# Performance work log

Measured on AMD Instinct MI355X. Metric: run time of the kernel, lower is better.

## Reference

```python
import jax, jax.numpy as jnp
import numpy as np

B, T, F, H, O = 256, 128, 128, 1024, 128


def setup_inputs() -> dict:
    key = jax.random.key(0)
    ks = jax.random.split(key, 16)
    s = 0.02  # small init scale to keep gates in a sane range
    return {
        "batch": jax.random.normal(ks[0], (B, T, F), jnp.float32),
        "Wih0": jax.random.normal(ks[1], (4 * H, F), jnp.float32) * s,
        "Whh0": jax.random.normal(ks[2], (4 * H, H), jnp.float32) * s,
        "bih0": jax.random.normal(ks[3], (4 * H,), jnp.float32) * s,
        "bhh0": jax.random.normal(ks[4], (4 * H,), jnp.float32) * s,
        "Wih1": jax.random.normal(ks[5], (4 * H, H), jnp.float32) * s,
        "Whh1": jax.random.normal(ks[6], (4 * H, H), jnp.float32) * s,
        "bih1": jax.random.normal(ks[7], (4 * H,), jnp.float32) * s,
        "bhh1": jax.random.normal(ks[8], (4 * H,), jnp.float32) * s,
        "h00": jax.random.normal(ks[9], (B, H), jnp.float32) * s,
        "c00": jax.random.normal(ks[10], (B, H), jnp.float32) * s,
        "h01": jax.random.normal(ks[11], (B, H), jnp.float32) * s,
        "c01": jax.random.normal(ks[12], (B, H), jnp.float32) * s,
        "Wout": jax.random.normal(ks[13], (O, T * H), jnp.float32) * 0.01,
        "bout": jax.random.normal(ks[14], (O,), jnp.float32) * 0.01,
    }


def _lstm_cell(x, h, c, Wih, Whh, bih, bhh):
    # torch.nn.LSTMCell: gates = x @ Wih.T + bih + h @ Whh.T + bhh, chunks i,f,g,o
    gates = x @ Wih.T + bih + h @ Whh.T + bhh  # [B, 4H]
    i, f, g, o = jnp.split(gates, 4, axis=-1)
    c_new = jax.nn.sigmoid(f) * c + jax.nn.sigmoid(i) * jnp.tanh(g)
    h_new = jax.nn.sigmoid(o) * jnp.tanh(c_new)
    return h_new, c_new


def reference(batch, Wih0, Whh0, bih0, bhh0, Wih1, Whh1, bih1, bhh1,
              h00, c00, h01, c01, Wout, bout):
    # Faithful to original: batch.view(T, B, -1) is a pure RESHAPE, not transpose.
    x = batch.reshape(T, B, F)

    def step(carry, xt):
        h0, c0, h1, c1 = carry
        h0, c0 = _lstm_cell(xt, h0, c0, Wih0, Whh0, bih0, bhh0)
        h1, c1 = _lstm_cell(h0, h1, c1, Wih1, Whh1, bih1, bhh1)
        return (h0, c0, h1, c1), h1

    _, outs = jax.lax.scan(step, (h00, c00, h01, c01), x)  # outs: [T, B, H]
    # Faithful: io.view(B, T, -1) then Flatten -> pure reshape to [B, T*H]
    flat = outs.reshape(B, T * H)
    return flat @ Wout.T + bout  # [B, O]
```

## Files before the change

### kernel.cpp

```cpp
#include <hip/hip_runtime.h>
#include <hip/hip_cooperative_groups.h>

namespace cg = cooperative_groups;

typedef __attribute__((ext_vector_type(8))) short short8;
typedef __attribute__((ext_vector_type(4))) float f32x4;

#define NBATCH 256
#define NSTEP  128
#define NFEAT  128
#define NHID   1024
#define NOUT   128
#define KOUT   131072
#define NBLK   256

#define W0H_OFF 0
#define W1_OFF  32768
#define CH_OFF  98304
#define SMEM_BYTES 163840

#define MFMA __builtin_amdgcn_mfma_f32_16x16x32_bf16

__device__ __forceinline__ unsigned short f2bf(float f){
  unsigned u = __float_as_uint(f);
  u += 0x7fffu + ((u >> 16) & 1u);
  return (unsigned short)(u >> 16);
}
__device__ __forceinline__ float sigf(float x){
  x = fminf(fmaxf(x, -30.f), 30.f);
  return 1.f / (1.f + __expf(-x));
}
__device__ __forceinline__ float tanhf_(float x){
  x = fminf(fmaxf(x, -15.f), 15.f);
  float e = __expf(2.f * x);
  return (e - 1.f) / (e + 1.f);
}

struct Params {
  const float *batch,*Wih0,*Whh0,*bih0,*bhh0,*Wih1,*Whh1,*bih1,*bhh1,*h00,*c00,*h01,*c01,*Wout,*bout;
  float *out;
  unsigned short *h0b,*h1b,*outs,*xbf;
  float *partial;
  unsigned *ctr;
};

__device__ __forceinline__ short8 ld8(const unsigned short* p){
  return *(const short8*)p;
}
__device__ __forceinline__ short8 ld8f(const float* p){
  f32x4 a = *(const f32x4*)p;
  f32x4 b = *(const f32x4*)(p + 4);
  short8 r;
  r[0]=(short)f2bf(a[0]); r[1]=(short)f2bf(a[1]); r[2]=(short)f2bf(a[2]); r[3]=(short)f2bf(a[3]);
  r[4]=(short)f2bf(b[0]); r[5]=(short)f2bf(b[1]); r[6]=(short)f2bf(b[2]); r[7]=(short)f2bf(b[3]);
  return r;
}

__device__ __forceinline__ void dma16(const void* g, void* l){
  __builtin_amdgcn_global_load_lds((const __attribute__((address_space(1))) unsigned int*)g,
                                   (__attribute__((address_space(3))) unsigned int*)l, 16, 0, 0);
}

__device__ __forceinline__ void slim_bar(unsigned* c, int tid){
  __syncthreads();
  if (tid == 0) {
    __builtin_amdgcn_fence(__ATOMIC_RELEASE, "agent");
    __hip_atomic_fetch_add(c, 1u, __ATOMIC_RELAXED, __HIP_MEMORY_SCOPE_AGENT);
    while (__hip_atomic_load(c, __ATOMIC_RELAXED, __HIP_MEMORY_SCOPE_AGENT) < (unsigned)NBLK)
      __builtin_amdgcn_s_sleep(2);
  }
  __syncthreads();
  __builtin_amdgcn_fence(__ATOMIC_ACQUIRE, "agent");
}

__global__ void __launch_bounds__(512, 2) lstm_all(Params a)
{
  extern __shared__ char smem[];
  const int bx = blockIdx.x, tid = threadIdx.x;
  const int gtid = bx * 512 + tid, nthr = gridDim.x * 512;
  const int w = tid >> 6, l = tid & 63, lo = l & 15, hi = l >> 4;
  const int klane = hi * 8;
  const int dR  = l >> 2;
  const int dgo = (((l & 3) ^ ((l >> 3) & 3)) & 3) * 8;

  if (bx == 0) for (int i = tid; i < 192; i += 512) a.ctr[i] = 0;
  for (int item = tid; item < 128 * 16; item += 512) {
    int g = item >> 4, lr = item & 15;
    int r = 16 * bx + lr, orig = (r & 3) * NHID + (r >> 2);
    *(short8*)(smem + W0H_OFF + item * 16) = ld8f(a.Whh0 + (size_t)orig * NHID + g * 8);
  }
  for (int item = tid; item < 256 * 16; item += 512) {
    int g = item >> 4, lr = item & 15;
    int r = 16 * bx + lr, orig = (r & 3) * NHID + (r >> 2);
    int k = g * 8;
    const float* src = (k < NHID) ? a.Wih1 + (size_t)orig * NHID + k
                                  : a.Whh1 + (size_t)orig * NHID + (k - NHID);
    *(short8*)(smem + W1_OFF + item * 16) = ld8f(src);
  }
  short8 wx[4];
  {
    int r = 16 * bx + lo, orig = (r & 3) * NHID + (r >> 2);
    const float* s = a.Wih0 + (size_t)orig * NFEAT + klane;
    #pragma unroll
    for (int i = 0; i < 4; i++) wx[i] = ld8f(s + i * 32);
  }
  for (int i = gtid; i < NBATCH * NHID; i += nthr) {
    a.h0b[NBATCH * NHID + i] = f2bf(a.h00[i]);
    a.h1b[NBATCH * NHID + i] = f2bf(a.h01[i]);
  }
  for (int i = gtid; i < NSTEP * NBATCH * NFEAT / 8; i += nthr)
    *(short8*)(a.xbf + (size_t)i * 8) = ld8f(a.batch + (size_t)i * 8);

  const int j = 4 * bx + hi;
  float b0r[4], b1r[4];
  #pragma unroll
  for (int q = 0; q < 4; q++) {
    b0r[q] = a.bih0[q * NHID + j] + a.bhh0[q * NHID + j];
    b1r[q] = a.bih1[q * NHID + j] + a.bhh1[q * NHID + j];
  }
  const int m0 = w * 32 + lo, m1 = m0 + 16;
  float c0r[2], c1r[2];
  c0r[0] = a.c00[(size_t)m0 * NHID + j]; c0r[1] = a.c00[(size_t)m1 * NHID + j];
  c1r[0] = a.c01[(size_t)m0 * NHID + j]; c1r[1] = a.c01[(size_t)m1 * NHID + j];
  __syncthreads();
  cg::this_grid().sync();

  const int rdo = lo * 64 + ((hi ^ ((lo >> 1) & 3)) << 4);
  for (int p = 0; p <= NSTEP; p++) {
    const int wpar = p & 1, rp = wpar ^ 1;
    const unsigned short* h0p = a.h0b + (size_t)rp   * NBATCH * NHID;
    const unsigned short* h1p = a.h1b + (size_t)wpar * NBATCH * NHID;
    const int t0 = (p < NSTEP) ? p : (NSTEP - 1);
    const unsigned short* xA  = a.xbf + (size_t)t0 * NBATCH * NFEAT + (size_t)(w * 32 + dR) * NFEAT + dgo;
    const unsigned short* h0A = h0p + (size_t)(w * 32 + dR) * NHID + dgo;
    const unsigned short* h1A = h1p + (size_t)(w * 32 + dR) * NHID + dgo;

    auto issue = [&](int cc){
      char* base = smem + CH_OFF + (cc & 3) * 16384 + w * 2048;
      if (cc < 4) {
        int ko = cc * 32;
        dma16(xA + ko, base); dma16(xA + 16 * NFEAT + ko, base + 1024);
      } else if (cc < 36) {
        int ko = (cc - 4) * 32;
        dma16(h0A + ko, base); dma16(h0A + 16 * NHID + ko, base + 1024);
      } else {
        int ko = (cc - 36) * 32;
        dma16(h1A + ko, base); dma16(h1A + 16 * NHID + ko, base + 1024);
      }
    };

    f32x4 l0a0 = {0.f,0.f,0.f,0.f}, l0a1 = {0.f,0.f,0.f,0.f};
    f32x4 l1a0 = {0.f,0.f,0.f,0.f}, l1a1 = {0.f,0.f,0.f,0.f};

    issue(0); issue(1); issue(2);

    #pragma unroll
    for (int c = 0; c < 68; ++c) {
      if      (c <= 65) asm volatile("s_waitcnt vmcnt(4)\n\ts_barrier" ::: "memory");
      else if (c == 66) asm volatile("s_waitcnt vmcnt(2)\n\ts_barrier" ::: "memory");
      else              asm volatile("s_waitcnt vmcnt(0)\n\ts_barrier" ::: "memory");
      if (c + 3 < 68) issue(c + 3);

      const char* cb = smem + CH_OFF + (c & 3) * 16384 + w * 2048;
      short8 a0 = *(const short8*)(cb + rdo);
      short8 a1 = *(const short8*)(cb + 1024 + rdo);

      if (c < 4) {
        l0a0 = MFMA(wx[c], a0, l0a0, 0,0,0); l0a1 = MFMA(wx[c], a1, l0a1, 0,0,0);
      } else if (c < 36) {
        int g = (c - 4) * 4 + hi;
        short8 w0f = *(const short8*)(smem + W0H_OFF + g * 256 + lo * 16);
        short8 w1f = *(const short8*)(smem + W1_OFF  + g * 256 + lo * 16);
        l0a0 = MFMA(w0f, a0, l0a0, 0,0,0); l0a1 = MFMA(w0f, a1, l0a1, 0,0,0);
        l1a0 = MFMA(w1f, a0, l1a0, 0,0,0); l1a1 = MFMA(w1f, a1, l1a1, 0,0,0);
      } else {
        int g = 128 + (c - 36) * 4 + hi;
        short8 wf = *(const short8*)(smem + W1_OFF + g * 256 + lo * 16);
        l1a0 = MFMA(wf, a0, l1a0, 0,0,0); l1a1 = MFMA(wf, a1, l1a1, 0,0,0);
      }
    }

    if (p < NSTEP) {
      unsigned short* ho = a.h0b + (size_t)wpar * NBATCH * NHID;
      float cn0 = sigf(l0a0[1] + b0r[1]) * c0r[0] + sigf(l0a0[0] + b0r[0]) * tanhf_(l0a0[2] + b0r[2]);
      c0r[0] = cn0;
      ho[(size_t)m0 * NHID + j] = f2bf(sigf(l0a0[3] + b0r[3]) * tanhf_(cn0));
      float cn1 = sigf(l0a1[1] + b0r[1]) * c0r[1] + sigf(l0a1[0] + b0r[0]) * tanhf_(l0a1[2] + b0r[2]);
      c0r[1] = cn1;
      ho[(size_t)m1 * NHID + j] = f2bf(sigf(l0a1[3] + b0r[3]) * tanhf_(cn1));
    }
    if (p >= 1) {
      unsigned short* h1o = a.h1b + (size_t)rp * NBATCH * NHID;
      unsigned short* oo  = a.outs + (size_t)(p - 1) * NBATCH * NHID;
      float cn0 = sigf(l1a0[1] + b1r[1]) * c1r[0] + sigf(l1a0[0] + b1r[0]) * tanhf_(l1a0[2] + b1r[2]);
      c1r[0] = cn0;
      unsigned short u0 = f2bf(sigf(l1a0[3] + b1r[3]) * tanhf_(cn0));
      h1o[(size_t)m0 * NHID + j] = u0; oo[(size_t)m0 * NHID + j] = u0;
      float cn1 = sigf(l1a1[1] + b1r[1]) * c1r[1] + sigf(l1a1[0] + b1r[0]) * tanhf_(l1a1[2] + b1r[2]);
      c1r[1] = cn1;
      unsigned short u1 = f2bf(sigf(l1a1[3] + b1r[3]) * tanhf_(cn1));
      h1o[(size_t)m1 * NHID + j] = u1; oo[(size_t)m1 * NHID + j] = u1;
    }
    slim_bar(a.ctr + p, tid);
  }

  cg::this_grid().sync();

  {
    int fnt = bx & 3, kc = bx >> 2;
    f32x4 facc[2][2];
    #pragma unroll
    for (int i = 0; i < 2; i++) { facc[i][0] = (f32x4)(0.f); facc[i][1] = (f32x4)(0.f); }
    const int kbase = kc * 2048;
    #pragma unroll 2
    for (int kk = 0; kk < 64; kk++) {
      short8 wf0 = ld8f(a.Wout + (size_t)(fnt * 32 +  0 + lo) * KOUT + kbase + kk * 32 + klane);
      short8 wf1 = ld8f(a.Wout + (size_t)(fnt * 32 + 16 + lo) * KOUT + kbase + kk * 32 + klane);
      #pragma unroll
      for (int mf = 0; mf < 2; mf++) {
        const unsigned short* ip = a.outs + (size_t)((w * 2 + mf) * 16 + lo) * KOUT + kbase + kk * 32 + klane;
        short8 af = ld8(ip);
        facc[mf][0] = MFMA(wf0, af, facc[mf][0], 0,0,0);
        facc[mf][1] = MFMA(wf1, af, facc[mf][1], 0,0,0);
      }
    }
    #pragma unroll
    for (int mf = 0; mf < 2; mf++)
      #pragma unroll
      for (int nf = 0; nf < 2; nf++)
        #pragma unroll
        for (int r = 0; r < 4; r++) {
          int o_loc = nf * 16 + 4 * hi + r;
          int i = (w * 2 + mf) * 16 + lo;
          a.partial[(size_t)(kc * 4 + fnt) * 8192 + o_loc * 256 + i] = facc[mf][nf][r];
        }
  }
  cg::this_grid().sync();

  for (int idx = gtid; idx < NBATCH * NOUT; idx += nthr) {
    int i = idx >> 7, o = idx & 127;
    float s = a.bout[o];
    #pragma unroll 4
    for (int kc2 = 0; kc2 < 64; kc2++)
      s += a.partial[(size_t)(kc2 * 4 + (o >> 5)) * 8192 + (o & 31) * 256 + i];
    a.out[idx] = s;
  }
}

extern "C" void kernel_launch(void* const* d_in, const int* in_sizes, int n_in,
                              void* d_out, int out_size, void* d_ws, size_t ws_size,
                              hipStream_t stream)
{
  (void)in_sizes; (void)n_in; (void)out_size; (void)ws_size;
  Params a;
  a.batch = (const float*)d_in[0];  a.Wih0 = (const float*)d_in[1];
  a.Whh0  = (const float*)d_in[2];  a.bih0 = (const float*)d_in[3];
  a.bhh0  = (const float*)d_in[4];  a.Wih1 = (const float*)d_in[5];
  a.Whh1  = (const float*)d_in[6];  a.bih1 = (const float*)d_in[7];
  a.bhh1  = (const float*)d_in[8];  a.h00  = (const float*)d_in[9];
  a.c00   = (const float*)d_in[10]; a.h01  = (const float*)d_in[11];
  a.c01   = (const float*)d_in[12]; a.Wout = (const float*)d_in[13];
  a.bout  = (const float*)d_in[14];
  a.out   = (float*)d_out;

  char* ws = (char*)d_ws;
  size_t off = 0;
  auto carve = [&](size_t bytes) { char* p = ws + off; off += (bytes + 255) & ~(size_t)255; return p; };
  a.h0b     = (unsigned short*)carve((size_t)2 * NBATCH * NHID * 2);
  a.h1b     = (unsigned short*)carve((size_t)2 * NBATCH * NHID * 2);
  a.outs    = (unsigned short*)carve((size_t)NSTEP * NBATCH * NHID * 2);
  a.xbf     = (unsigned short*)carve((size_t)NSTEP * NBATCH * NFEAT * 2);
  a.partial = (float*)carve((size_t)256 * 8192 * 4);
  a.ctr     = (unsigned*)carve((size_t)256 * 4);

  hipFuncSetAttribute((const void*)lstm_all, hipFuncAttributeMaxDynamicSharedMemorySize, SMEM_BYTES);

  void* kargs[] = { &a };
  hipLaunchCooperativeKernel((void*)lstm_all, dim3(256), dim3(512), kargs, SMEM_BYTES, stream);
}
```

Measured before the change: 5.527 ms.

## Replace LDS DMA staging of activations with direct register prefetch pipeline

Drops the global_load_lds ring buffer in shared memory, along with its per-chunk waitcnt and s_barrier sync. Each wave now loads its own A fragments straight from global memory into a register ring that runs 7 chunks ahead. This cuts LDS use and the block-wide barriers inside the hot loop. The cost is more VGPRs for the 16 prefetched short8 values, compiler-managed wait counts, and possibly less coalesced global loads. Occupancy is pinned to 2 waves per EU.

```diff
diff --git a/kernel.cpp b/kernel.cpp
--- a/kernel.cpp
+++ b/kernel.cpp
@@ -16,8 +16,7 @@
 
 #define W0H_OFF 0
 #define W1_OFF  32768
-#define CH_OFF  98304
-#define SMEM_BYTES 163840
+#define SMEM_BYTES 98304
 
 #define MFMA __builtin_amdgcn_mfma_f32_16x16x32_bf16
 
@@ -56,11 +55,6 @@
   return r;
 }
 
-__device__ __forceinline__ void dma16(const void* g, void* l){
-  __builtin_amdgcn_global_load_lds((const __attribute__((address_space(1))) unsigned int*)g,
-                                   (__attribute__((address_space(3))) unsigned int*)l, 16, 0, 0);
-}
-
 __device__ __forceinline__ void slim_bar(unsigned* c, int tid){
   __syncthreads();
   if (tid == 0) {
@@ -73,15 +67,14 @@
   __builtin_amdgcn_fence(__ATOMIC_ACQUIRE, "agent");
 }
 
-__global__ void __launch_bounds__(512, 2) lstm_all(Params a)
+__attribute__((amdgpu_waves_per_eu(2, 2)))
+__global__ void __launch_bounds__(512) lstm_all(Params a)
 {
   extern __shared__ char smem[];
   const int bx = blockIdx.x, tid = threadIdx.x;
   const int gtid = bx * 512 + tid, nthr = gridDim.x * 512;
   const int w = tid >> 6, l = tid & 63, lo = l & 15, hi = l >> 4;
   const int klane = hi * 8;
-  const int dR  = l >> 2;
-  const int dgo = (((l & 3) ^ ((l >> 3) & 3)) & 3) * 8;
 
   if (bx == 0) for (int i = tid; i < 192; i += 512) a.ctr[i] = 0;
   for (int item = tid; item < 128 * 16; item += 512) {
@@ -125,45 +118,41 @@
   __syncthreads();
   cg::this_grid().sync();
 
-  const int rdo = lo * 64 + ((hi ^ ((lo >> 1) & 3)) << 4);
   for (int p = 0; p <= NSTEP; p++) {
     const int wpar = p & 1, rp = wpar ^ 1;
     const unsigned short* h0p = a.h0b + (size_t)rp   * NBATCH * NHID;
     const unsigned short* h1p = a.h1b + (size_t)wpar * NBATCH * NHID;
     const int t0 = (p < NSTEP) ? p : (NSTEP - 1);
-    const unsigned short* xA  = a.xbf + (size_t)t0 * NBATCH * NFEAT + (size_t)(w * 32 + dR) * NFEAT + dgo;
-    const unsigned short* h0A = h0p + (size_t)(w * 32 + dR) * NHID + dgo;
-    const unsigned short* h1A = h1p + (size_t)(w * 32 + dR) * NHID + dgo;
-
-    auto issue = [&](int cc){
-      char* base = smem + CH_OFF + (cc & 3) * 16384 + w * 2048;
-      if (cc < 4) {
-        int ko = cc * 32;
-        dma16(xA + ko, base); dma16(xA + 16 * NFEAT + ko, base + 1024);
-      } else if (cc < 36) {
-        int ko = (cc - 4) * 32;
-        dma16(h0A + ko, base); dma16(h0A + 16 * NHID + ko, base + 1024);
-      } else {
-        int ko = (cc - 36) * 32;
-        dma16(h1A + ko, base); dma16(h1A + 16 * NHID + ko, base + 1024);
-      }
+    const unsigned short* xP0  = a.xbf + (size_t)t0 * NBATCH * NFEAT + (size_t)m0 * NFEAT + klane;
+    const unsigned short* xP1  = xP0 + (size_t)16 * NFEAT;
+    const unsigned short* h0P0 = h0p + (size_t)m0 * NHID + klane;
+    const unsigned short* h0P1 = h0P0 + (size_t)16 * NHID;
+    const unsigned short* h1P0 = h1p + (size_t)m0 * NHID + klane;
+    const unsigned short* h1P1 = h1P0 + (size_t)16 * NHID;
+
+    auto lda0 = [&](int cc){
+      return (cc < 4) ? ld8(xP0 + cc * 32)
+           : (cc < 36) ? ld8(h0P0 + (cc - 4) * 32)
+                       : ld8(h1P0 + (cc - 36) * 32);
+    };
+    auto lda1 = [&](int cc){
+      return (cc < 4) ? ld8(xP1 + cc * 32)
+           : (cc < 36) ? ld8(h0P1 + (cc - 4) * 32)
+                       : ld8(h1P1 + (cc - 36) * 32);
     };
 
     f32x4 l0a0 = {0.f,0.f,0.f,0.f}, l0a1 = {0.f,0.f,0.f,0.f};
     f32x4 l1a0 = {0.f,0.f,0.f,0.f}, l1a1 = {0.f,0.f,0.f,0.f};
 
-    issue(0); issue(1); issue(2);
+    short8 ra[8], rb[8];
+    #pragma unroll
+    for (int q = 0; q < 7; q++) { ra[q] = lda0(q); rb[q] = lda1(q); }
 
     #pragma unroll
     for (int c = 0; c < 68; ++c) {
-      if      (c <= 65) asm volatile("s_waitcnt vmcnt(4)\n\ts_barrier" ::: "memory");
-      else if (c == 66) asm volatile("s_waitcnt vmcnt(2)\n\ts_barrier" ::: "memory");
-      else              asm volatile("s_waitcnt vmcnt(0)\n\ts_barrier" ::: "memory");
-      if (c + 3 < 68) issue(c + 3);
-
-      const char* cb = smem + CH_OFF + (c & 3) * 16384 + w * 2048;
-      short8 a0 = *(const short8*)(cb + rdo);
-      short8 a1 = *(const short8*)(cb + 1024 + rdo);
+      if (c + 7 < 68) { ra[(c + 7) & 7] = lda0(c + 7); rb[(c + 7) & 7] = lda1(c + 7); }
+      short8 a0 = ra[c & 7];
+      short8 a1 = rb[c & 7];
 
       if (c < 4) {
         l0a0 = MFMA(wx[c], a0, l0a0, 0,0,0); l0a1 = MFMA(wx[c], a1, l0a1, 0,0,0);
```

Result: slower. 8.210 ms (+48.5%).

## Double waves per block and give each wave a private DMA ring without barriers

Applied to the files above, without the earlier changes.

Each block now runs 1024 threads (16 waves), and each wave owns 16 batch rows instead of 32. The per-step MFMA chain per wave is halved, and the output projection is split the same way. Each wave gets its own 4-slot LDS ring for the x/h0/h1 chunks, so the block-wide s_barrier in the K loop is replaced by a per-wave vmcnt wait. The aim is to shorten the latency-bound critical path of each recurrent step. The cost is register pressure under 1024-thread launch bounds and more waves contending for LDS and the global barrier.

```diff
diff --git a/kernel.cpp b/kernel.cpp
--- a/kernel.cpp
+++ b/kernel.cpp
@@ -73,23 +73,23 @@
   __builtin_amdgcn_fence(__ATOMIC_ACQUIRE, "agent");
 }
 
-__global__ void __launch_bounds__(512, 2) lstm_all(Params a)
+__global__ void __launch_bounds__(1024, 4) lstm_all(Params a)
 {
   extern __shared__ char smem[];
   const int bx = blockIdx.x, tid = threadIdx.x;
-  const int gtid = bx * 512 + tid, nthr = gridDim.x * 512;
+  const int gtid = bx * 1024 + tid, nthr = gridDim.x * 1024;
   const int w = tid >> 6, l = tid & 63, lo = l & 15, hi = l >> 4;
   const int klane = hi * 8;
   const int dR  = l >> 2;
   const int dgo = (((l & 3) ^ ((l >> 3) & 3)) & 3) * 8;
 
-  if (bx == 0) for (int i = tid; i < 192; i += 512) a.ctr[i] = 0;
-  for (int item = tid; item < 128 * 16; item += 512) {
+  if (bx == 0) for (int i = tid; i < 192; i += 1024) a.ctr[i] = 0;
+  for (int item = tid; item < 128 * 16; item += 1024) {
     int g = item >> 4, lr = item & 15;
     int r = 16 * bx + lr, orig = (r & 3) * NHID + (r >> 2);
     *(short8*)(smem + W0H_OFF + item * 16) = ld8f(a.Whh0 + (size_t)orig * NHID + g * 8);
   }
-  for (int item = tid; item < 256 * 16; item += 512) {
+  for (int item = tid; item < 256 * 16; item += 1024) {
     int g = item >> 4, lr = item & 15;
     int r = 16 * bx + lr, orig = (r & 3) * NHID + (r >> 2);
     int k = g * 8;
@@ -112,94 +112,78 @@
     *(short8*)(a.xbf + (size_t)i * 8) = ld8f(a.batch + (size_t)i * 8);
 
   const int j = 4 * bx + hi;
+  const int m0 = w * 16 + lo;
   float b0r[4], b1r[4];
   #pragma unroll
   for (int q = 0; q < 4; q++) {
     b0r[q] = a.bih0[q * NHID + j] + a.bhh0[q * NHID + j];
     b1r[q] = a.bih1[q * NHID + j] + a.bhh1[q * NHID + j];
   }
-  const int m0 = w * 32 + lo, m1 = m0 + 16;
-  float c0r[2], c1r[2];
-  c0r[0] = a.c00[(size_t)m0 * NHID + j]; c0r[1] = a.c00[(size_t)m1 * NHID + j];
-  c1r[0] = a.c01[(size_t)m0 * NHID + j]; c1r[1] = a.c01[(size_t)m1 * NHID + j];
+  float c0r = a.c00[(size_t)m0 * NHID + j];
+  float c1r = a.c01[(size_t)m0 * NHID + j];
   __syncthreads();
   cg::this_grid().sync();
 
+  char* ring = smem + CH_OFF + w * 4096;
   const int rdo = lo * 64 + ((hi ^ ((lo >> 1) & 3)) << 4);
   for (int p = 0; p <= NSTEP; p++) {
     const int wpar = p & 1, rp = wpar ^ 1;
     const unsigned short* h0p = a.h0b + (size_t)rp   * NBATCH * NHID;
     const unsigned short* h1p = a.h1b + (size_t)wpar * NBATCH * NHID;
     const int t0 = (p < NSTEP) ? p : (NSTEP - 1);
-    const unsigned short* xA  = a.xbf + (size_t)t0 * NBATCH * NFEAT + (size_t)(w * 32 + dR) * NFEAT + dgo;
-    const unsigned short* h0A = h0p + (size_t)(w * 32 + dR) * NHID + dgo;
-    const unsigned short* h1A = h1p + (size_t)(w * 32 + dR) * NHID + dgo;
+    const unsigned short* xA  = a.xbf + (size_t)t0 * NBATCH * NFEAT + (size_t)(w * 16 + dR) * NFEAT + dgo;
+    const unsigned short* h0A = h0p + (size_t)(w * 16 + dR) * NHID + dgo;
+    const unsigned short* h1A = h1p + (size_t)(w * 16 + dR) * NHID + dgo;
 
     auto issue = [&](int cc){
-      char* base = smem + CH_OFF + (cc & 3) * 16384 + w * 2048;
-      if (cc < 4) {
-        int ko = cc * 32;
-        dma16(xA + ko, base); dma16(xA + 16 * NFEAT + ko, base + 1024);
-      } else if (cc < 36) {
-        int ko = (cc - 4) * 32;
-        dma16(h0A + ko, base); dma16(h0A + 16 * NHID + ko, base + 1024);
-      } else {
-        int ko = (cc - 36) * 32;
-        dma16(h1A + ko, base); dma16(h1A + 16 * NHID + ko, base + 1024);
-      }
+      char* base = ring + (cc & 3) * 1024;
+      if      (cc < 4)  dma16(xA  + cc * 32,        base);
+      else if (cc < 36) dma16(h0A + (cc - 4) * 32,  base);
+      else              dma16(h1A + (cc - 36) * 32, base);
     };
 
-    f32x4 l0a0 = {0.f,0.f,0.f,0.f}, l0a1 = {0.f,0.f,0.f,0.f};
-    f32x4 l1a0 = {0.f,0.f,0.f,0.f}, l1a1 = {0.f,0.f,0.f,0.f};
+    f32x4 l0a0 = {0.f,0.f,0.f,0.f};
+    f32x4 l1a0 = {0.f,0.f,0.f,0.f};
 
     issue(0); issue(1); issue(2);
 
     #pragma unroll
     for (int c = 0; c < 68; ++c) {
-      if      (c <= 65) asm volatile("s_waitcnt vmcnt(4)\n\ts_barrier" ::: "memory");
-      else if (c == 66) asm volatile("s_waitcnt vmcnt(2)\n\ts_barrier" ::: "memory");
-      else              asm volatile("s_waitcnt vmcnt(0)\n\ts_barrier" ::: "memory");
+      if      (c <= 65) asm volatile("s_waitcnt vmcnt(2)" ::: "memory");
+      else if (c == 66) asm volatile("s_waitcnt vmcnt(1)" ::: "memory");
+      else              asm volatile("s_waitcnt vmcnt(0)" ::: "memory");
       if (c + 3 < 68) issue(c + 3);
 
-      const char* cb = smem + CH_OFF + (c & 3) * 16384 + w * 2048;
-      short8 a0 = *(const short8*)(cb + rdo);
-      short8 a1 = *(const short8*)(cb + 1024 + rdo);
+      short8 a0 = *(const short8*)(ring + (c & 3) * 1024 + rdo);
 
       if (c < 4) {
-        l0a0 = MFMA(wx[c], a0, l0a0, 0,0,0); l0a1 = MFMA(wx[c], a1, l0a1, 0,0,0);
+        l0a0 = MFMA(wx[c], a0, l0a0, 0,0,0);
       } else if (c < 36) {
         int g = (c - 4) * 4 + hi;
         short8 w0f = *(const short8*)(smem + W0H_OFF + g * 256 + lo * 16);
         short8 w1f = *(const short8*)(smem + W1_OFF  + g * 256 + lo * 16);
-        l0a0 = MFMA(w0f, a0, l0a0, 0,0,0); l0a1 = MFMA(w0f, a1, l0a1, 0,0,0);
-        l1a0 = MFMA(w1f, a0, l1a0, 0,0,0); l1a1 = MFMA(w1f, a1, l1a1, 0,0,0);
+        l0a0 = MFMA(w0f, a0, l0a0, 0,0,0);
+        l1a0 = MFMA(w1f, a0, l1a0, 0,0,0);
       } else {
         int g = 128 + (c - 36) * 4 + hi;
         short8 wf = *(const short8*)(smem + W1_OFF + g * 256 + lo * 16);
-        l1a0 = MFMA(wf, a0, l1a0, 0,0,0); l1a1 = MFMA(wf, a1, l1a1, 0,0,0);
+        l1a0 = MFMA(wf, a0, l1a0, 0,0,0);
       }
     }
 
     if (p < NSTEP) {
       unsigned short* ho = a.h0b + (size_t)wpar * NBATCH * NHID;
-      float cn0 = sigf(l0a0[1] + b0r[1]) * c0r[0] + sigf(l0a0[0] + b0r[0]) * tanhf_(l0a0[2] + b0r[2]);
-      c0r[0] = cn0;
-      ho[(size_t)m0 * NHID + j] = f2bf(sigf(l0a0[3] + b0r[3]) * tanhf_(cn0));
-      float cn1 = sigf(l0a1[1] + b0r[1]) * c0r[1] + sigf(l0a1[0] + b0r[0]) * tanhf_(l0a1[2] + b0r[2]);
-      c0r[1] = cn1;
-      ho[(size_t)m1 * NHID + j] = f2bf(sigf(l0a1[3] + b0r[3]) * tanhf_(cn1));
+      float cn = sigf(l0a0[1] + b0r[1]) * c0r + sigf(l0a0[0] + b0r[0]) * tanhf_(l0a0[2] + b0r[2]);
+      c0r = cn;
+      ho[(size_t)m0 * NHID + j] = f2bf(sigf(l0a0[3] + b0r[3]) * tanhf_(cn));
     }
     if (p >= 1) {
       unsigned short* h1o = a.h1b + (size_t)rp * NBATCH * NHID;
       unsigned short* oo  = a.outs + (size_t)(p - 1) * NBATCH * NHID;
-      float cn0 = sigf(l1a0[1] + b1r[1]) * c1r[0] + sigf(l1a0[0] + b1r[0]) * tanhf_(l1a0[2] + b1r[2]);
-      c1r[0] = cn0;
-      unsigned short u0 = f2bf(sigf(l1a0[3] + b1r[3]) * tanhf_(cn0));
-      h1o[(size_t)m0 * NHID + j] = u0; oo[(size_t)m0 * NHID + j] = u0;
-      float cn1 = sigf(l1a1[1] + b1r[1]) * c1r[1] + sigf(l1a1[0] + b1r[0]) * tanhf_(l1a1[2] + b1r[2]);
-      c1r[1] = cn1;
-      unsigned short u1 = f2bf(sigf(l1a1[3] + b1r[3]) * tanhf_(cn1));
-      h1o[(size_t)m1 * NHID + j] = u1; oo[(size_t)m1 * NHID + j] = u1;
+      float cn = sigf(l1a0[1] + b1r[1]) * c1r + sigf(l1a0[0] + b1r[0]) * tanhf_(l1a0[2] + b1r[2]);
+      c1r = cn;
+      unsigned short u = f2bf(sigf(l1a0[3] + b1r[3]) * tanhf_(cn));
+      h1o[(size_t)m0 * NHID + j] = u; oo[(size_t)m0 * NHID + j] = u;
     }
     slim_bar(a.ctr + p, tid);
   }
@@ -208,32 +192,26 @@
 
   {
     int fnt = bx & 3, kc = bx >> 2;
-    f32x4 facc[2][2];
-    #pragma unroll
-    for (int i = 0; i < 2; i++) { facc[i][0] = (f32x4)(0.f); facc[i][1] = (f32x4)(0.f); }
+    f32x4 facc[2];
+    facc[0] = (f32x4)(0.f); facc[1] = (f32x4)(0.f);
     const int kbase = kc * 2048;
     #pragma unroll 2
     for (int kk = 0; kk < 64; kk++) {
       short8 wf0 = ld8f(a.Wout + (size_t)(fnt * 32 +  0 + lo) * KOUT + kbase + kk * 32 + klane);
       short8 wf1 = ld8f(a.Wout + (size_t)(fnt * 32 + 16 + lo) * KOUT + kbase + kk * 32 + klane);
+      const unsigned short* ip = a.outs + (size_t)(w * 16 + lo) * KOUT + kbase + kk * 32 + klane;
+      short8 af = ld8(ip);
+      facc[0] = MFMA(wf0, af, facc[0], 0,0,0);
+      facc[1] = MFMA(wf1, af, facc[1], 0,0,0);
+    }
+    #pragma unroll
+    for (int nf = 0; nf < 2; nf++)
       #pragma unroll
-      for (int mf = 0; mf < 2; mf++) {
-        const unsigned short* ip = a.outs + (size_t)((w * 2 + mf) * 16 + lo) * KOUT + kbase + kk * 32 + klane;
-        short8 af = ld8(ip);
-        facc[mf][0] = MFMA(wf0, af, facc[mf][0], 0,0,0);
-        facc[mf][1] = MFMA(wf1, af, facc[mf][1], 0,0,0);
+      for (int r = 0; r < 4; r++) {
+        int o_loc = nf * 16 + 4 * hi + r;
+        int i = w * 16 + lo;
+        a.partial[(size_t)(kc * 4 + fnt) * 8192 + o_loc * 256 + i] = facc[nf][r];
       }
-    }
-    #pragma unroll
-    for (int mf = 0; mf < 2; mf++)
-      #pragma unroll
-      for (int nf = 0; nf < 2; nf++)
-        #pragma unroll
-        for (int r = 0; r < 4; r++) {
-          int o_loc = nf * 16 + 4 * hi + r;
-          int i = (w * 2 + mf) * 16 + lo;
-          a.partial[(size_t)(kc * 4 + fnt) * 8192 + o_loc * 256 + i] = facc[mf][nf][r];
-        }
   }
   cg::this_grid().sync();
 
@@ -276,5 +254,5 @@
   hipFuncSetAttribute((const void*)lstm_all, hipFuncAttributeMaxDynamicSharedMemorySize, SMEM_BYTES);
 
   void* kargs[] = { &a };
-  hipLaunchCooperativeKernel((void*)lstm_all, dim3(256), dim3(512), kargs, SMEM_BYTES, stream);
-}
+  hipLaunchCooperativeKernel((void*)lstm_all, dim3(256), dim3(1024), kargs, SMEM_BYTES, stream);
+}
```

Result: slower. 7.122 ms (+28.8%).

## Use two-level tree grid barrier and packed 8-byte hidden-state stores

Applied to the files above, without the earlier changes.

Replaces the per-step flat grid barrier, where all 256 blocks hit one atomic counter, with a two-level barrier. Blocks first count into 16 group counters padded onto separate cache lines, and the last arriver of each group bumps a root counter that everyone polls. Hidden-state outputs are packed four bf16 values per lane via cross-lane shuffles and written as a single 8-byte agent-scope atomic store, cutting the number of scattered 2-byte global stores. The release fence is replaced by an explicit vmcnt wait, and all blocks now zero a larger counter array at startup, which leans on timing before the first barrier.

```diff
diff --git a/kernel.cpp b/kernel.cpp
--- a/kernel.cpp
+++ b/kernel.cpp
@@ -19,6 +19,9 @@
 #define CH_OFF  98304
 #define SMEM_BYTES 163840
 
+#define CTR_STRIDE 272
+#define CTR_TOTAL  (129 * CTR_STRIDE)
+
 #define MFMA __builtin_amdgcn_mfma_f32_16x16x32_bf16
 
 __device__ __forceinline__ unsigned short f2bf(float f){
@@ -61,13 +64,25 @@
                                    (__attribute__((address_space(3))) unsigned int*)l, 16, 0, 0);
 }
 
-__device__ __forceinline__ void slim_bar(unsigned* c, int tid){
+__device__ __forceinline__ unsigned long long pack4(unsigned short u){
+  unsigned v = (unsigned)u | ((unsigned)(unsigned short)__shfl_xor((int)(unsigned)u, 16) << 16);
+  unsigned hi32 = (unsigned)__shfl_xor((int)v, 32);
+  return (unsigned long long)v | ((unsigned long long)hi32 << 32);
+}
+__device__ __forceinline__ void st8a(unsigned short* p, unsigned long long v){
+  __hip_atomic_store((unsigned long long*)p, v, __ATOMIC_RELAXED, __HIP_MEMORY_SCOPE_AGENT);
+}
+
+__device__ __forceinline__ void tree_bar(unsigned* base, int bx, int tid){
+  asm volatile("s_waitcnt vmcnt(0)" ::: "memory");
   __syncthreads();
   if (tid == 0) {
-    __builtin_amdgcn_fence(__ATOMIC_RELEASE, "agent");
-    __hip_atomic_fetch_add(c, 1u, __ATOMIC_RELAXED, __HIP_MEMORY_SCOPE_AGENT);
-    while (__hip_atomic_load(c, __ATOMIC_RELAXED, __HIP_MEMORY_SCOPE_AGENT) < (unsigned)NBLK)
-      __builtin_amdgcn_s_sleep(2);
+    unsigned old = __hip_atomic_fetch_add(base + (bx & 15) * 16, 1u,
+                                          __ATOMIC_RELAXED, __HIP_MEMORY_SCOPE_AGENT);
+    if (old == 15u)
+      __hip_atomic_fetch_add(base + 256, 1u, __ATOMIC_RELAXED, __HIP_MEMORY_SCOPE_AGENT);
+    while (__hip_atomic_load(base + 256, __ATOMIC_RELAXED, __HIP_MEMORY_SCOPE_AGENT) < 16u)
+      __builtin_amdgcn_s_sleep(1);
   }
   __syncthreads();
   __builtin_amdgcn_fence(__ATOMIC_ACQUIRE, "agent");
@@ -83,7 +98,7 @@
   const int dR  = l >> 2;
   const int dgo = (((l & 3) ^ ((l >> 3) & 3)) & 3) * 8;
 
-  if (bx == 0) for (int i = tid; i < 192; i += 512) a.ctr[i] = 0;
+  for (int i = gtid; i < CTR_TOTAL; i += nthr) a.ctr[i] = 0;
   for (int item = tid; item < 128 * 16; item += 512) {
     int g = item >> 4, lr = item & 15;
     int r = 16 * bx + lr, orig = (r & 3) * NHID + (r >> 2);
@@ -184,24 +199,34 @@
       unsigned short* ho = a.h0b + (size_t)wpar * NBATCH * NHID;
       float cn0 = sigf(l0a0[1] + b0r[1]) * c0r[0] + sigf(l0a0[0] + b0r[0]) * tanhf_(l0a0[2] + b0r[2]);
       c0r[0] = cn0;
-      ho[(size_t)m0 * NHID + j] = f2bf(sigf(l0a0[3] + b0r[3]) * tanhf_(cn0));
+      unsigned short hb0 = f2bf(sigf(l0a0[3] + b0r[3]) * tanhf_(cn0));
       float cn1 = sigf(l0a1[1] + b0r[1]) * c0r[1] + sigf(l0a1[0] + b0r[0]) * tanhf_(l0a1[2] + b0r[2]);
       c0r[1] = cn1;
-      ho[(size_t)m1 * NHID + j] = f2bf(sigf(l0a1[3] + b0r[3]) * tanhf_(cn1));
+      unsigned short hb1 = f2bf(sigf(l0a1[3] + b0r[3]) * tanhf_(cn1));
+      unsigned long long pk0 = pack4(hb0), pk1 = pack4(hb1);
+      if (hi == 0) {
+        st8a(ho + (size_t)m0 * NHID + 4 * bx, pk0);
+        st8a(ho + (size_t)m1 * NHID + 4 * bx, pk1);
+      }
     }
     if (p >= 1) {
       unsigned short* h1o = a.h1b + (size_t)rp * NBATCH * NHID;
       unsigned short* oo  = a.outs + (size_t)(p - 1) * NBATCH * NHID;
       float cn0 = sigf(l1a0[1] + b1r[1]) * c1r[0] + sigf(l1a0[0] + b1r[0]) * tanhf_(l1a0[2] + b1r[2]);
       c1r[0] = cn0;
-      unsigned short u0 = f2bf(sigf(l1a0[3] + b1r[3]) * tanhf_(cn0));
-      h1o[(size_t)m0 * NHID + j] = u0; oo[(size_t)m0 * NHID + j] = u0;
+      unsigned short hb0 = f2bf(sigf(l1a0[3] + b1r[3]) * tanhf_(cn0));
       float cn1 = sigf(l1a1[1] + b1r[1]) * c1r[1] + sigf(l1a1[0] + b1r[0]) * tanhf_(l1a1[2] + b1r[2]);
       c1r[1] = cn1;
-      unsigned short u1 = f2bf(sigf(l1a1[3] + b1r[3]) * tanhf_(cn1));
-      h1o[(size_t)m1 * NHID + j] = u1; oo[(size_t)m1 * NHID + j] = u1;
+      unsigned short hb1 = f2bf(sigf(l1a1[3] + b1r[3]) * tanhf_(cn1));
+      unsigned long long pk0 = pack4(hb0), pk1 = pack4(hb1);
+      if (hi == 0) {
+        st8a(h1o + (size_t)m0 * NHID + 4 * bx, pk0);
+        st8a(h1o + (size_t)m1 * NHID + 4 * bx, pk1);
+        st8a(oo  + (size_t)m0 * NHID + 4 * bx, pk0);
+        st8a(oo  + (size_t)m1 * NHID + 4 * bx, pk1);
+      }
     }
-    slim_bar(a.ctr + p, tid);
+    tree_bar(a.ctr + p * CTR_STRIDE, bx, tid);
   }
 
   cg::this_grid().sync();
@@ -271,7 +296,7 @@
   a.outs    = (unsigned short*)carve((size_t)NSTEP * NBATCH * NHID * 2);
   a.xbf     = (unsigned short*)carve((size_t)NSTEP * NBATCH * NFEAT * 2);
   a.partial = (float*)carve((size_t)256 * 8192 * 4);
-  a.ctr     = (unsigned*)carve((size_t)256 * 4);
+  a.ctr     = (unsigned*)carve((size_t)CTR_TOTAL * 4);
 
   hipFuncSetAttribute((const void*)lstm_all, hipFuncAttributeMaxDynamicSharedMemorySize, SMEM_BYTES);
 
```

New measurement: 4.991 ms. -9.7%, faster.
